# Performance work log

Measured on AMD Instinct MI355X. Metric: run time of the kernel, lower is better.

The kernel has to match this reference:

```python
import jax, jax.numpy as jnp
import numpy as np

B, N, DIM, H = 8, 1024, 768, 12
D = DIM // H  # head_dim = 64
SCALE = D ** -0.5


def setup_inputs() -> dict:
    key = jax.random.key(0)
    k1, k2, k3, k4 = jax.random.split(key, 4)
    x = jax.random.normal(k1, (B, N, DIM), dtype=jnp.float32)
    # nn.Linear(dim, dim*3, bias=False): weight [3*dim, dim]; y = x @ W^T
    w_qkv = jax.random.normal(k2, (3 * DIM, DIM), dtype=jnp.float32) * (DIM ** -0.5)
    # nn.Linear(dim, dim) with bias
    w_proj = jax.random.normal(k3, (DIM, DIM), dtype=jnp.float32) * (DIM ** -0.5)
    b_proj = jax.random.normal(k4, (DIM,), dtype=jnp.float32) * 0.01
    return {"x": x, "w_qkv": w_qkv, "w_proj": w_proj, "b_proj": b_proj}


def reference(x, w_qkv, w_proj, b_proj):
    b, n, dim = x.shape
    qkv = x @ w_qkv.T  # [b, n, 3*dim]
    # rearrange 'b n (h d qkv) -> qkv b h n d' (qkv innermost in the split)
    qkv = qkv.reshape(b, n, H, D, 3)
    qkv = jnp.transpose(qkv, (4, 0, 2, 1, 3))  # [3, b, h, n, d]
    q, k, v = qkv[0], qkv[1], qkv[2]
    energy = jnp.einsum('bhqd,bhkd->bhqk', q, k) * SCALE
    att = jax.nn.softmax(energy, axis=-1)  # dropout p=0.0 -> identity
    out = jnp.einsum('bhal,bhlv->bhav', att, v)  # [b, h, n, d]
    out = jnp.transpose(out, (0, 2, 1, 3)).reshape(b, n, dim)
    return out @ w_proj.T + b_proj
```

## Files before the change

kernel.cpp:

```cpp
#include <hip/hip_runtime.h>
#include <hip/hip_bf16.h>
#include <stdint.h>

#define NH 12

typedef __attribute__((ext_vector_type(8))) short bf16x8;
typedef __attribute__((ext_vector_type(4))) float f32x4;

static __device__ __forceinline__ ushort f2bf(float f) {
  union { float f; uint32_t u; } v; v.f = f;
  uint32_t r = (v.u + 0x7FFFu + ((v.u >> 16) & 1u)) >> 16;
  return (ushort)r;
}

static __device__ __forceinline__ uint32_t cvtpk(float lo, float hi) {
  uint32_t r;
  asm("v_cvt_pk_bf16_f32 %0, %1, %2" : "=v"(r) : "v"(lo), "v"(hi));
  return r;
}

static __device__ __forceinline__ void gl_lds16(const void* g, void* l) {
  __builtin_amdgcn_global_load_lds(
      (const __attribute__((address_space(1))) uint32_t*)(uintptr_t)g,
      (__attribute__((address_space(3))) uint32_t*)(uintptr_t)l,
      16, 0, 0);
}

static __device__ __forceinline__ f32x4 mfma32(bf16x8 a, bf16x8 b, f32x4 c) {
  return __builtin_amdgcn_mfma_f32_16x16x32_bf16(a, b, c, 0, 0, 0);
}

#define QSCALE 0.1803368801111601f

#define N4_X  1572864
#define N4_WQ 442368
#define N4_WP 147456
__global__ __launch_bounds__(256) void k_cvt_all(const float4* __restrict__ X,
                                                 const float4* __restrict__ Wq,
                                                 const float4* __restrict__ Wp,
                                                 ushort4* __restrict__ Xb,
                                                 ushort4* __restrict__ Wqb,
                                                 ushort4* __restrict__ Wpb) {
  int i = blockIdx.x * 256 + threadIdx.x;
  if (i < N4_X) {
    float4 v = X[i];
    ushort4 o;
    o.x = f2bf(v.x); o.y = f2bf(v.y); o.z = f2bf(v.z); o.w = f2bf(v.w);
    Xb[i] = o;
  } else if (i < N4_X + N4_WQ) {
    int j = i - N4_X;
    int ro = j / 192, cc = j - ro * 192;
    int h = ro / 192;
    int rem = ro - h * 192;
    int d = rem / 3;
    int which = rem - d * 3;
    int rn = which * 768 + h * 64 + d;
    float4 v = Wq[j];
    ushort4 o;
    o.x = f2bf(v.x); o.y = f2bf(v.y); o.z = f2bf(v.z); o.w = f2bf(v.w);
    Wqb[(size_t)rn * 192 + cc] = o;
  } else {
    int j = i - N4_X - N4_WQ;
    float4 v = Wp[j];
    ushort4 o;
    o.x = f2bf(v.x); o.y = f2bf(v.y); o.z = f2bf(v.z); o.w = f2bf(v.w);
    Wpb[j] = o;
  }
}

#define DECL_GEMM_VARS() \
  const int tid = threadIdx.x; \
  const int w = tid >> 6, l = tid & 63, g = l >> 4, c15 = l & 15; \
  const int wm = w >> 1, wn = w & 1; \
  const int dst0 = w * 1024 + l * 16; \
  const int row_s = w * 16 + (l >> 2); \
  const int cg = ((l & 3) ^ ((l >> 3) & 3)) * 8; \
  const int gsw = (g ^ ((c15 >> 1) & 3)) * 8;

#define STAGE(pa, pb, Aptr, Bptr, kk0) do { \
    gl_lds16((Aptr) + (size_t)(m0 + row_s) * 768 + (kk0) + cg, (char*)(pa) + dst0); \
    gl_lds16((Aptr) + (size_t)(m0 + row_s + 64) * 768 + (kk0) + cg, (char*)(pa) + dst0 + 4096); \
    gl_lds16((Bptr) + (size_t)(n0 + row_s) * 768 + (kk0) + cg, (char*)(pb) + dst0); \
    gl_lds16((Bptr) + (size_t)(n0 + row_s + 64) * 768 + (kk0) + cg, (char*)(pb) + dst0 + 4096); \
  } while (0)

#define COMPUTE(pa, pb) do { \
    bf16x8 af[4], bfr[4]; \
    _Pragma("unroll") \
    for (int i = 0; i < 4; i++) { \
      af[i]  = *(const bf16x8*)&(pa)[(wm * 64 + i * 16 + c15) * 32 + gsw]; \
      bfr[i] = *(const bf16x8*)&(pb)[(wn * 64 + i * 16 + c15) * 32 + gsw]; \
    } \
    _Pragma("unroll") \
    for (int mr = 0; mr < 4; mr++) \
      _Pragma("unroll") \
      for (int nr = 0; nr < 4; nr++) \
        acc[mr][nr] = mfma32(af[mr], bfr[nr], acc[mr][nr]); \
  } while (0)

#define WB4 do { __builtin_amdgcn_sched_barrier(0); \
    asm volatile("s_waitcnt vmcnt(4)\n\ts_barrier" ::: "memory"); \
    __builtin_amdgcn_sched_barrier(0); } while (0)
#define WB2 do { __builtin_amdgcn_sched_barrier(0); \
    asm volatile("s_waitcnt vmcnt(2)\n\ts_barrier" ::: "memory"); \
    __builtin_amdgcn_sched_barrier(0); } while (0)
#define WB0 do { __builtin_amdgcn_sched_barrier(0); \
    asm volatile("s_waitcnt vmcnt(0)\n\ts_barrier" ::: "memory"); \
    __builtin_amdgcn_sched_barrier(0); } while (0)
#define PFENCE do { asm volatile("" ::: "memory"); \
    __builtin_amdgcn_sched_barrier(0); } while (0)

#define GEMM_PIPE(Aptr, Bptr) do { \
    STAGE(A0, B0, Aptr, Bptr, 0); \
    PFENCE; \
    STAGE(A1, B1, Aptr, Bptr, 32); \
    WB4; \
    _Pragma("unroll 1") \
    for (int k0 = 0; k0 < 672; k0 += 96) { \
      STAGE(A2, B2, Aptr, Bptr, k0 + 64);  COMPUTE(A0, B0); WB4; \
      STAGE(A0, B0, Aptr, Bptr, k0 + 96);  COMPUTE(A1, B1); WB4; \
      STAGE(A1, B1, Aptr, Bptr, k0 + 128); COMPUTE(A2, B2); WB4; \
    } \
    STAGE(A2, B2, Aptr, Bptr, 736); COMPUTE(A0, B0); WB4; \
    COMPUTE(A1, B1); WB0; \
    COMPUTE(A2, B2); \
  } while (0)

__global__ __launch_bounds__(256, 3) void k_qkv(const ushort* __restrict__ X,
                                                const ushort* __restrict__ W,
                                                ushort* __restrict__ Qb,
                                                ushort* __restrict__ Kf,
                                                ushort* __restrict__ Vf) {
  __shared__ __align__(16) ushort lds[24576];
  const int id = (int)blockIdx.x;
  const int swz = (id & 7) * 144 + (id >> 3);
  const int bx = swz % 18, by = swz / 18;
  const int m0 = by * 128, n0 = bx * 128;
  DECL_GEMM_VARS();

  ushort* A0 = lds;
  ushort* A1 = lds + 4096;
  ushort* A2 = lds + 8192;
  ushort* B0 = lds + 12288;
  ushort* B1 = lds + 16384;
  ushort* B2 = lds + 20480;

  f32x4 acc[4][4] = {};
  GEMM_PIPE(X, W);
  __syncthreads();

  const int type = bx / 6;
  const int cb = (bx % 6) * 128;
  const int h0 = cb >> 6;
  const int b = m0 >> 10, nbase = m0 & 1023, tbase = nbase >> 5;

  if (type == 0) {
#pragma unroll
    for (int nr = 0; nr < 4; nr++) {
      const int colrel = wn * 64 + nr * 16 + c15;
#pragma unroll
      for (int mr = 0; mr < 4; mr++)
#pragma unroll
        for (int r = 0; r < 4; r++) {
          const int mrel = wm * 64 + mr * 16 + 4 * g + r;
          lds[mrel * 128 + colrel] = f2bf(acc[mr][nr][r] * QSCALE);
        }
    }
    __syncthreads();
#pragma unroll
    for (int j = 0; j < 8; j++) {
      const int cid = j * 256 + tid;
      const int n = cid >> 4, coloff = (cid & 15) * 8;
      const int hrel = coloff >> 6, d0q = coloff & 63;
      bf16x8 vv = *(const bf16x8*)&lds[n * 128 + coloff];
      *(bf16x8*)(Qb + ((size_t)(b * NH + h0 + hrel) * 1024 + nbase + n) * 64 + d0q) = vv;
    }
  } else if (type == 1) {
#pragma unroll
    for (int nr = 0; nr < 4; nr++) {
      const int colrel = wn * 64 + nr * 16 + c15;
      const int hrel = colrel >> 6, d = colrel & 63;
      const int gk = (d >> 3) & 3, ek = d & 7, hi = d >> 5;
#pragma unroll
      for (int mr = 0; mr < 4; mr++)
#pragma unroll
        for (int r = 0; r < 4; r++) {
          const int mrel = wm * 64 + mr * 16 + 4 * g + r;
          const int trel = mrel >> 5, kk = mrel & 31;
          const int x = kk >> 3, s = (kk >> 2) & 1, y = kk & 3;
          lds[(hrel * 4 + trel) * 2048 + (2 * s + hi) * 512 +
              (gk * 16 + x * 4 + y) * 8 + ek] = f2bf(acc[mr][nr][r]);
        }
    }
    __syncthreads();
    const int c = tid >> 5, jj = tid & 31;
    ushort* dst = Kf + ((size_t)(b * NH + h0 + (c >> 2)) * 32 + tbase + (c & 3)) * 2048;
    const ushort* srcl = lds + c * 2048;
#pragma unroll
    for (int k2 = 0; k2 < 8; k2++)
      *(bf16x8*)(dst + jj * 8 + k2 * 256) = *(const bf16x8*)(srcl + jj * 8 + k2 * 256);
  } else {
#pragma unroll
    for (int nr = 0; nr < 4; nr++) {
      const int colrel = wn * 64 + nr * 16 + c15;
      const int hrel = colrel >> 6, d = colrel & 63;
      const int dtv = d >> 4, cv = d & 15;
#pragma unroll
      for (int mr = 0; mr < 4; mr++)
#pragma unroll
        for (int r = 0; r < 4; r++) {
          const int mrel = wm * 64 + mr * 16 + 4 * g + r;
          const int trel = mrel >> 5, kk = mrel & 31;
          const int gv = kk >> 3, ev = kk & 7;
          lds[(hrel * 4 + trel) * 2048 + dtv * 512 +
              (gv * 16 + cv) * 8 + ev] = f2bf(acc[mr][nr][r]);
        }
    }
    __syncthreads();
    const int c = tid >> 5, jj = tid & 31;
    ushort* dst = Vf + ((size_t)(b * NH + h0 + (c >> 2)) * 32 + tbase + (c & 3)) * 2048;
    const ushort* srcl = lds + c * 2048;
#pragma unroll
    for (int k2 = 0; k2 < 8; k2++)
      *(bf16x8*)(dst + jj * 8 + k2 * 256) = *(const bf16x8*)(srcl + jj * 8 + k2 * 256);
  }
}

__global__ __launch_bounds__(256, 3) void k_attn(const ushort* __restrict__ Qb,
                                                 const ushort* __restrict__ Kf,
                                                 const ushort* __restrict__ Vf,
                                                 ushort* __restrict__ Ab) {
  __shared__ __align__(16) ushort kv[3][4096];
  const int bh = blockIdx.x;
  const int tid = threadIdx.x;
  const int w = tid >> 6, l = tid & 63, g = l >> 4, c15 = l & 15;
  const int q0 = blockIdx.y * 128 + w * 32;

  bf16x8 qf0a, qf0b, qf1a, qf1b;
  {
    const ushort* qp = Qb + ((size_t)bh * 1024 + q0 + c15) * 64 + g * 8;
    qf0a = *(const bf16x8*)qp;
    qf0b = *(const bf16x8*)(qp + 32);
    qf1a = *(const bf16x8*)(qp + 1024);
    qf1b = *(const bf16x8*)(qp + 1024 + 32);
  }
  const ushort* kgb = Kf + (size_t)bh * 32 * 2048;
  const ushort* vgb = Vf + (size_t)bh * 32 * 2048;

  bf16x8 vones;
#pragma unroll
  for (int j = 0; j < 8; j++) vones[j] = (short)0x3F80;

  f32x4 o0[4] = {}, o1[4] = {};
  f32x4 ol0 = {}, ol1 = {};

#define STAGE_KV(bi, t) do { \
    gl_lds16(kgb + (size_t)(t) * 2048 + tid * 8, (char*)kv[bi] + tid * 16); \
    gl_lds16(vgb + (size_t)(t) * 2048 + tid * 8, (char*)kv[bi] + 4096 + tid * 16); \
  } while (0)

#define ATT_BODY(bi) do { \
    const ushort* kp = kv[bi] + l * 8; \
    const ushort* vp = kv[bi] + 2048 + l * 8; \
    bf16x8 ka0a = *(const bf16x8*)(kp); \
    bf16x8 ka0b = *(const bf16x8*)(kp + 512); \
    bf16x8 ka1a = *(const bf16x8*)(kp + 1024); \
    bf16x8 ka1b = *(const bf16x8*)(kp + 1536); \
    f32x4 s00 = {0.f,0.f,0.f,0.f}, s01 = {0.f,0.f,0.f,0.f}; \
    f32x4 s10 = {0.f,0.f,0.f,0.f}, s11 = {0.f,0.f,0.f,0.f}; \
    s00 = mfma32(ka0a, qf0a, s00); s00 = mfma32(ka0b, qf0b, s00); \
    s01 = mfma32(ka0a, qf1a, s01); s01 = mfma32(ka0b, qf1b, s01); \
    s10 = mfma32(ka1a, qf0a, s10); s10 = mfma32(ka1b, qf0b, s10); \
    s11 = mfma32(ka1a, qf1a, s11); s11 = mfma32(ka1b, qf1b, s11); \
    float p0[8], p1[8]; \
    _Pragma("unroll") \
    for (int r = 0; r < 4; r++) { \
      p0[r]     = exp2f(s00[r]); \
      p0[4 + r] = exp2f(s10[r]); \
      p1[r]     = exp2f(s01[r]); \
      p1[4 + r] = exp2f(s11[r]); \
    } \
    union { uint32_t u[4]; bf16x8 v; } pa0, pa1; \
    _Pragma("unroll") \
    for (int j = 0; j < 4; j++) { \
      pa0.u[j] = cvtpk(p0[2 * j], p0[2 * j + 1]); \
      pa1.u[j] = cvtpk(p1[2 * j], p1[2 * j + 1]); \
    } \
    ol0 = mfma32(pa0.v, vones, ol0); \
    ol1 = mfma32(pa1.v, vones, ol1); \
    _Pragma("unroll") \
    for (int dt = 0; dt < 4; dt++) { \
      bf16x8 vb = *(const bf16x8*)(vp + dt * 512); \
      o0[dt] = mfma32(pa0.v, vb, o0[dt]); \
      o1[dt] = mfma32(pa1.v, vb, o1[dt]); \
    } \
  } while (0)

  STAGE_KV(0, 0);
  PFENCE;
  STAGE_KV(1, 1);
  WB2;
#pragma unroll 1
  for (int t = 0; t < 27; t += 3) {
    STAGE_KV(2, t + 2); ATT_BODY(0); WB2;
    STAGE_KV(0, t + 3); ATT_BODY(1); WB2;
    STAGE_KV(1, t + 4); ATT_BODY(2); WB2;
  }
  STAGE_KV(2, 29); ATT_BODY(0); WB2;
  STAGE_KV(0, 30); ATT_BODY(1); WB2;
  STAGE_KV(1, 31); ATT_BODY(2); WB2;
  ATT_BODY(0); WB0;
  ATT_BODY(1);
#undef ATT_BODY
#undef STAGE_KV

  float il0[4], il1[4];
#pragma unroll
  for (int r = 0; r < 4; r++) {
    il0[r] = __builtin_amdgcn_rcpf(ol0[r]);
    il1[r] = __builtin_amdgcn_rcpf(ol1[r]);
  }
  const int b = bh / NH, h = bh % NH;
#pragma unroll
  for (int dt = 0; dt < 4; dt++)
#pragma unroll
    for (int r = 0; r < 4; r++) {
      const int n = q0 + 4 * g + r;
      Ab[(size_t)(b * 1024 + n) * 768 + h * 64 + dt * 16 + c15] =
          f2bf(o0[dt][r] * il0[r]);
      Ab[(size_t)(b * 1024 + n + 16) * 768 + h * 64 + dt * 16 + c15] =
          f2bf(o1[dt][r] * il1[r]);
    }
}

__global__ __launch_bounds__(256, 3) void k_proj(const ushort* __restrict__ Ain,
                                                 const ushort* __restrict__ W,
                                                 const float* __restrict__ Bp,
                                                 float* __restrict__ Out) {
  __shared__ __align__(16) ushort lds[24576];
  const int id = (int)blockIdx.x;
  const int swz = (id & 7) * 48 + (id >> 3);
  const int bx = swz % 6, by = swz / 6;
  const int m0 = by * 128, n0 = bx * 128;
  DECL_GEMM_VARS();

  ushort* A0 = lds;
  ushort* A1 = lds + 4096;
  ushort* A2 = lds + 8192;
  ushort* B0 = lds + 12288;
  ushort* B1 = lds + 16384;
  ushort* B2 = lds + 20480;

  f32x4 acc[4][4] = {};
  GEMM_PIPE(Ain, W);

#pragma unroll
  for (int nr = 0; nr < 4; nr++) {
    const int cc = n0 + wn * 64 + nr * 16 + c15;
    const float bias = Bp[cc];
#pragma unroll
    for (int mr = 0; mr < 4; mr++) {
      const int mb = m0 + wm * 64 + mr * 16 + 4 * g;
#pragma unroll
      for (int r = 0; r < 4; r++) {
        const int m = mb + r;
        Out[(size_t)m * 768 + cc] = acc[mr][nr][r] + bias;
      }
    }
  }
}

extern "C" void kernel_launch(void* const* d_in, const int* in_sizes, int n_in,
                              void* d_out, int out_size, void* d_ws, size_t ws_size,
                              hipStream_t stream) {
  const float* X  = (const float*)d_in[0];
  const float* Wq = (const float*)d_in[1];
  const float* Wp = (const float*)d_in[2];
  const float* Bp = (const float*)d_in[3];
  float* Out = (float*)d_out;

  char* ws = (char*)d_ws;
  const size_t SZ = (size_t)96 * 1024 * 64 * sizeof(ushort);
  ushort* Qb  = (ushort*)(ws);
  ushort* Kf  = (ushort*)(ws + SZ);
  ushort* Vf  = (ushort*)(ws + 2 * SZ);
  ushort* Ab  = (ushort*)(ws + 3 * SZ);
  ushort* Xb  = (ushort*)(ws + 4 * SZ);
  ushort* Wqb = (ushort*)(ws + 5 * SZ);
  ushort* Wpb = (ushort*)(ws + 5 * SZ + 2304 * 768 * 2);

  k_cvt_all<<<(N4_X + N4_WQ + N4_WP) / 256, 256, 0, stream>>>(
      (const float4*)X, (const float4*)Wq, (const float4*)Wp,
      (ushort4*)Xb, (ushort4*)Wqb, (ushort4*)Wpb);

  k_qkv<<<1152, 256, 0, stream>>>(Xb, Wqb, Qb, Kf, Vf);
  k_attn<<<dim3(96, 8), 256, 0, stream>>>(Qb, Kf, Vf, Ab);
  k_proj<<<384, 256, 0, stream>>>(Ab, Wpb, Bp, Out);
}
```

Measured before the change: 108.6 us.

## Load A fragments directly to registers and quad-buffer B in LDS

The two GEMM kernels now load the A operand straight from global memory into register fragments with double-buffered registers, and stage only the B operand into LDS through a 4-slot ring. This shrinks LDS per block from 48KB to 32KB, and launch bounds are raised to 4 blocks per CU. The aim is to cut LDS traffic and raise occupancy. In exchange, the direct A loads are 16-byte per-lane global loads with a 1536-byte row stride, so they coalesce less well and hide latency less. Register pressure also rises from holding the extra fragments.

Measured after the change: 175.6 us. 61.7% more time.

```diff
diff --git a/kernel.cpp b/kernel.cpp
--- a/kernel.cpp
+++ b/kernel.cpp
@@ -77,20 +77,24 @@
   const int cg = ((l & 3) ^ ((l >> 3) & 3)) * 8; \
   const int gsw = (g ^ ((c15 >> 1) & 3)) * 8;
 
-#define STAGE(pa, pb, Aptr, Bptr, kk0) do { \
-    gl_lds16((Aptr) + (size_t)(m0 + row_s) * 768 + (kk0) + cg, (char*)(pa) + dst0); \
-    gl_lds16((Aptr) + (size_t)(m0 + row_s + 64) * 768 + (kk0) + cg, (char*)(pa) + dst0 + 4096); \
-    gl_lds16((Bptr) + (size_t)(n0 + row_s) * 768 + (kk0) + cg, (char*)(pb) + dst0); \
-    gl_lds16((Bptr) + (size_t)(n0 + row_s + 64) * 768 + (kk0) + cg, (char*)(pb) + dst0 + 4096); \
-  } while (0)
-
-#define COMPUTE(pa, pb) do { \
-    bf16x8 af[4], bfr[4]; \
-    _Pragma("unroll") \
-    for (int i = 0; i < 4; i++) { \
-      af[i]  = *(const bf16x8*)&(pa)[(wm * 64 + i * 16 + c15) * 32 + gsw]; \
-      bfr[i] = *(const bf16x8*)&(pb)[(wn * 64 + i * 16 + c15) * 32 + gsw]; \
-    } \
+#define B_STAGE(bi, Bptr, kk0) do { \
+    char* _b = (char*)lds + (bi) * 8192; \
+    gl_lds16((Bptr) + (size_t)(n0 + row_s) * 768 + (kk0) + cg, _b + dst0); \
+    gl_lds16((Bptr) + (size_t)(n0 + row_s + 64) * 768 + (kk0) + cg, _b + dst0 + 4096); \
+  } while (0)
+
+#define A_LOAD(af, Aptr, kk0) do { \
+    _Pragma("unroll") \
+    for (int i = 0; i < 4; i++) \
+      af[i] = *(const bf16x8*)((Aptr) + (size_t)(m0 + wm * 64 + i * 16 + c15) * 768 + (kk0) + g * 8); \
+  } while (0)
+
+#define COMPUTE2(af, bi) do { \
+    const ushort* _bb = lds + (bi) * 4096; \
+    bf16x8 bfr[4]; \
+    _Pragma("unroll") \
+    for (int i = 0; i < 4; i++) \
+      bfr[i] = *(const bf16x8*)&_bb[(wn * 64 + i * 16 + c15) * 32 + gsw]; \
     _Pragma("unroll") \
     for (int mr = 0; mr < 4; mr++) \
       _Pragma("unroll") \
@@ -98,6 +102,9 @@
         acc[mr][nr] = mfma32(af[mr], bfr[nr], acc[mr][nr]); \
   } while (0)
 
+#define WB6 do { __builtin_amdgcn_sched_barrier(0); \
+    asm volatile("s_waitcnt vmcnt(6)\n\ts_barrier" ::: "memory"); \
+    __builtin_amdgcn_sched_barrier(0); } while (0)
 #define WB4 do { __builtin_amdgcn_sched_barrier(0); \
     asm volatile("s_waitcnt vmcnt(4)\n\ts_barrier" ::: "memory"); \
     __builtin_amdgcn_sched_barrier(0); } while (0)
@@ -110,43 +117,43 @@
 #define PFENCE do { asm volatile("" ::: "memory"); \
     __builtin_amdgcn_sched_barrier(0); } while (0)
 
-#define GEMM_PIPE(Aptr, Bptr) do { \
-    STAGE(A0, B0, Aptr, Bptr, 0); \
-    PFENCE; \
-    STAGE(A1, B1, Aptr, Bptr, 32); \
+#define GEMM_PIPE2(Aptr, Bptr) do { \
+    B_STAGE(0, Bptr, 0); PFENCE; \
+    B_STAGE(1, Bptr, 32); PFENCE; \
+    A_LOAD(afA, Aptr, 0); PFENCE; \
+    _Pragma("unroll 1") \
+    for (int p = 0; p < 22; p += 2) { \
+      B_STAGE((p + 2) & 3, Bptr, (p + 2) * 32); \
+      A_LOAD(afB, Aptr, (p + 1) * 32); \
+      WB6; \
+      COMPUTE2(afA, p & 3); \
+      B_STAGE((p + 3) & 3, Bptr, (p + 3) * 32); \
+      A_LOAD(afA, Aptr, (p + 2) * 32); \
+      WB6; \
+      COMPUTE2(afB, (p + 1) & 3); \
+    } \
+    A_LOAD(afB, Aptr, 736); \
     WB4; \
-    _Pragma("unroll 1") \
-    for (int k0 = 0; k0 < 672; k0 += 96) { \
-      STAGE(A2, B2, Aptr, Bptr, k0 + 64);  COMPUTE(A0, B0); WB4; \
-      STAGE(A0, B0, Aptr, Bptr, k0 + 96);  COMPUTE(A1, B1); WB4; \
-      STAGE(A1, B1, Aptr, Bptr, k0 + 128); COMPUTE(A2, B2); WB4; \
-    } \
-    STAGE(A2, B2, Aptr, Bptr, 736); COMPUTE(A0, B0); WB4; \
-    COMPUTE(A1, B1); WB0; \
-    COMPUTE(A2, B2); \
-  } while (0)
-
-__global__ __launch_bounds__(256, 3) void k_qkv(const ushort* __restrict__ X,
+    COMPUTE2(afA, 2); \
+    WB0; \
+    COMPUTE2(afB, 3); \
+  } while (0)
+
+__global__ __launch_bounds__(256, 4) void k_qkv(const ushort* __restrict__ X,
                                                 const ushort* __restrict__ W,
                                                 ushort* __restrict__ Qb,
                                                 ushort* __restrict__ Kf,
                                                 ushort* __restrict__ Vf) {
-  __shared__ __align__(16) ushort lds[24576];
+  __shared__ __align__(16) ushort lds[16384];
   const int id = (int)blockIdx.x;
   const int swz = (id & 7) * 144 + (id >> 3);
   const int bx = swz % 18, by = swz / 18;
   const int m0 = by * 128, n0 = bx * 128;
   DECL_GEMM_VARS();
 
-  ushort* A0 = lds;
-  ushort* A1 = lds + 4096;
-  ushort* A2 = lds + 8192;
-  ushort* B0 = lds + 12288;
-  ushort* B1 = lds + 16384;
-  ushort* B2 = lds + 20480;
-
   f32x4 acc[4][4] = {};
-  GEMM_PIPE(X, W);
+  bf16x8 afA[4], afB[4];
+  GEMM_PIPE2(X, W);
   __syncthreads();
 
   const int type = bx / 6;
@@ -333,26 +340,20 @@
     }
 }
 
-__global__ __launch_bounds__(256, 3) void k_proj(const ushort* __restrict__ Ain,
+__global__ __launch_bounds__(256, 4) void k_proj(const ushort* __restrict__ Ain,
                                                  const ushort* __restrict__ W,
                                                  const float* __restrict__ Bp,
                                                  float* __restrict__ Out) {
-  __shared__ __align__(16) ushort lds[24576];
+  __shared__ __align__(16) ushort lds[16384];
   const int id = (int)blockIdx.x;
   const int swz = (id & 7) * 48 + (id >> 3);
   const int bx = swz % 6, by = swz / 6;
   const int m0 = by * 128, n0 = bx * 128;
   DECL_GEMM_VARS();
 
-  ushort* A0 = lds;
-  ushort* A1 = lds + 4096;
-  ushort* A2 = lds + 8192;
-  ushort* B0 = lds + 12288;
-  ushort* B1 = lds + 16384;
-  ushort* B2 = lds + 20480;
-
   f32x4 acc[4][4] = {};
-  GEMM_PIPE(Ain, W);
+  bf16x8 afA[4], afB[4];
+  GEMM_PIPE2(Ain, W);
 
 #pragma unroll
   for (int nr = 0; nr < 4; nr++) {
```

## Retile QKV GEMM to 256x128 blocks with 8 waves sharing B fragments

Applied to the files above, without the earlier changes.

The QKV projection kernel now uses 512-thread blocks that each compute a 256x128 output tile. Each of the 8 waves owns 32 rows and all 128 columns, so the B tile is loaded once per block and shared across more rows, halving the grid to 576 blocks. The staging pipeline is rewritten to move three 16-byte loads per thread per k-step, and the epilogue is adapted to the taller tile. LDS use grows to 72KB per block and each wave now issues more B-fragment LDS reads, which may limit occupancy. The attention kernel is only moved in the file, unchanged.

Measured after the change: 111.3 us. 1.02x slower.

```diff
diff --git a/kernel.cpp b/kernel.cpp
--- a/kernel.cpp
+++ b/kernel.cpp
@@ -68,38 +68,11 @@
   }
 }
 
-#define DECL_GEMM_VARS() \
-  const int tid = threadIdx.x; \
-  const int w = tid >> 6, l = tid & 63, g = l >> 4, c15 = l & 15; \
-  const int wm = w >> 1, wn = w & 1; \
-  const int dst0 = w * 1024 + l * 16; \
-  const int row_s = w * 16 + (l >> 2); \
-  const int cg = ((l & 3) ^ ((l >> 3) & 3)) * 8; \
-  const int gsw = (g ^ ((c15 >> 1) & 3)) * 8;
-
-#define STAGE(pa, pb, Aptr, Bptr, kk0) do { \
-    gl_lds16((Aptr) + (size_t)(m0 + row_s) * 768 + (kk0) + cg, (char*)(pa) + dst0); \
-    gl_lds16((Aptr) + (size_t)(m0 + row_s + 64) * 768 + (kk0) + cg, (char*)(pa) + dst0 + 4096); \
-    gl_lds16((Bptr) + (size_t)(n0 + row_s) * 768 + (kk0) + cg, (char*)(pb) + dst0); \
-    gl_lds16((Bptr) + (size_t)(n0 + row_s + 64) * 768 + (kk0) + cg, (char*)(pb) + dst0 + 4096); \
-  } while (0)
-
-#define COMPUTE(pa, pb) do { \
-    bf16x8 af[4], bfr[4]; \
-    _Pragma("unroll") \
-    for (int i = 0; i < 4; i++) { \
-      af[i]  = *(const bf16x8*)&(pa)[(wm * 64 + i * 16 + c15) * 32 + gsw]; \
-      bfr[i] = *(const bf16x8*)&(pb)[(wn * 64 + i * 16 + c15) * 32 + gsw]; \
-    } \
-    _Pragma("unroll") \
-    for (int mr = 0; mr < 4; mr++) \
-      _Pragma("unroll") \
-      for (int nr = 0; nr < 4; nr++) \
-        acc[mr][nr] = mfma32(af[mr], bfr[nr], acc[mr][nr]); \
-  } while (0)
-
 #define WB4 do { __builtin_amdgcn_sched_barrier(0); \
     asm volatile("s_waitcnt vmcnt(4)\n\ts_barrier" ::: "memory"); \
+    __builtin_amdgcn_sched_barrier(0); } while (0)
+#define WB3 do { __builtin_amdgcn_sched_barrier(0); \
+    asm volatile("s_waitcnt vmcnt(3)\n\ts_barrier" ::: "memory"); \
     __builtin_amdgcn_sched_barrier(0); } while (0)
 #define WB2 do { __builtin_amdgcn_sched_barrier(0); \
     asm volatile("s_waitcnt vmcnt(2)\n\ts_barrier" ::: "memory"); \
@@ -109,6 +82,283 @@
     __builtin_amdgcn_sched_barrier(0); } while (0)
 #define PFENCE do { asm volatile("" ::: "memory"); \
     __builtin_amdgcn_sched_barrier(0); } while (0)
+
+__global__ __launch_bounds__(512, 4) void k_qkv(const ushort* __restrict__ X,
+                                                const ushort* __restrict__ W,
+                                                ushort* __restrict__ Qb,
+                                                ushort* __restrict__ Kf,
+                                                ushort* __restrict__ Vf) {
+  __shared__ __align__(16) ushort lds[36864];
+  const int id = (int)blockIdx.x;
+  const int swz = (id & 7) * 72 + (id >> 3);
+  const int bx = swz % 18, by = swz / 18;
+  const int m0 = by * 256, n0 = bx * 128;
+  const int tid = threadIdx.x;
+  const int w = tid >> 6, l = tid & 63, g = l >> 4, c15 = l & 15;
+  const int rowA = tid >> 2;
+  const int cgA = ((tid & 3) ^ ((tid >> 3) & 3)) * 8;
+  const int gsw = (g ^ ((c15 >> 1) & 3)) * 8;
+
+#define A_BUF(i) ((char*)lds + (i) * 16384)
+#define B_BUF(i) ((char*)lds + 49152 + (i) * 8192)
+
+#define STAGE8(bi, kk0) do { \
+    gl_lds16(X + (size_t)(m0 + rowA) * 768 + (kk0) + cgA, A_BUF(bi) + tid * 16); \
+    gl_lds16(X + (size_t)(m0 + rowA + 128) * 768 + (kk0) + cgA, A_BUF(bi) + tid * 16 + 8192); \
+    gl_lds16(W + (size_t)(n0 + rowA) * 768 + (kk0) + cgA, B_BUF(bi) + tid * 16); \
+  } while (0)
+
+#define COMPUTE8(bi) do { \
+    const ushort* _a = (const ushort*)A_BUF(bi); \
+    const ushort* _b = (const ushort*)B_BUF(bi); \
+    bf16x8 af[2], bfr[8]; \
+    _Pragma("unroll") \
+    for (int i = 0; i < 2; i++) \
+      af[i] = *(const bf16x8*)&_a[(w * 32 + i * 16 + c15) * 32 + gsw]; \
+    _Pragma("unroll") \
+    for (int i = 0; i < 8; i++) \
+      bfr[i] = *(const bf16x8*)&_b[(i * 16 + c15) * 32 + gsw]; \
+    _Pragma("unroll") \
+    for (int mr = 0; mr < 2; mr++) \
+      _Pragma("unroll") \
+      for (int nr = 0; nr < 8; nr++) \
+        acc[mr][nr] = mfma32(af[mr], bfr[nr], acc[mr][nr]); \
+  } while (0)
+
+  f32x4 acc[2][8] = {};
+
+  STAGE8(0, 0);
+  PFENCE;
+  STAGE8(1, 32);
+  WB3;
+#pragma unroll 1
+  for (int p = 0; p < 21; p += 3) {
+    STAGE8(2, (p + 2) * 32); COMPUTE8(0); WB3;
+    STAGE8(0, (p + 3) * 32); COMPUTE8(1); WB3;
+    STAGE8(1, (p + 4) * 32); COMPUTE8(2); WB3;
+  }
+  STAGE8(2, 736); COMPUTE8(0); WB3;
+  COMPUTE8(1); WB0;
+  COMPUTE8(2);
+  __syncthreads();
+
+  const int type = bx / 6;
+  const int cb = (bx % 6) * 128;
+  const int h0 = cb >> 6;
+  const int b = m0 >> 10, nbase = m0 & 1023, tbase = nbase >> 5;
+
+  if (type == 0) {
+#pragma unroll
+    for (int nr = 0; nr < 8; nr++) {
+      const int colrel = nr * 16 + c15;
+#pragma unroll
+      for (int mr = 0; mr < 2; mr++)
+#pragma unroll
+        for (int r = 0; r < 4; r++) {
+          const int mrel = w * 32 + mr * 16 + 4 * g + r;
+          lds[mrel * 128 + colrel] = f2bf(acc[mr][nr][r] * QSCALE);
+        }
+    }
+    __syncthreads();
+#pragma unroll
+    for (int j = 0; j < 8; j++) {
+      const int cid = j * 512 + tid;
+      const int n = cid >> 4, coloff = (cid & 15) * 8;
+      const int hrel = coloff >> 6, d0q = coloff & 63;
+      bf16x8 vv = *(const bf16x8*)&lds[n * 128 + coloff];
+      *(bf16x8*)(Qb + ((size_t)(b * NH + h0 + hrel) * 1024 + nbase + n) * 64 + d0q) = vv;
+    }
+  } else if (type == 1) {
+#pragma unroll
+    for (int nr = 0; nr < 8; nr++) {
+      const int colrel = nr * 16 + c15;
+      const int hrel = colrel >> 6, d = colrel & 63;
+      const int gk = (d >> 3) & 3, ek = d & 7, hi = d >> 5;
+#pragma unroll
+      for (int mr = 0; mr < 2; mr++)
+#pragma unroll
+        for (int r = 0; r < 4; r++) {
+          const int mrel = w * 32 + mr * 16 + 4 * g + r;
+          const int trel = mrel >> 5, kk = mrel & 31;
+          const int x = kk >> 3, s = (kk >> 2) & 1, y = kk & 3;
+          lds[(hrel * 8 + trel) * 2048 + (2 * s + hi) * 512 +
+              (gk * 16 + x * 4 + y) * 8 + ek] = f2bf(acc[mr][nr][r]);
+        }
+    }
+    __syncthreads();
+    const int c = tid >> 5, jj = tid & 31;
+    ushort* dst = Kf + ((size_t)(b * NH + h0 + (c >> 3)) * 32 + tbase + (c & 7)) * 2048;
+    const ushort* srcl = lds + c * 2048;
+#pragma unroll
+    for (int k2 = 0; k2 < 8; k2++)
+      *(bf16x8*)(dst + jj * 8 + k2 * 256) = *(const bf16x8*)(srcl + jj * 8 + k2 * 256);
+  } else {
+#pragma unroll
+    for (int nr = 0; nr < 8; nr++) {
+      const int colrel = nr * 16 + c15;
+      const int hrel = colrel >> 6, d = colrel & 63;
+      const int dtv = d >> 4, cv = d & 15;
+#pragma unroll
+      for (int mr = 0; mr < 2; mr++)
+#pragma unroll
+        for (int r = 0; r < 4; r++) {
+          const int mrel = w * 32 + mr * 16 + 4 * g + r;
+          const int trel = mrel >> 5, kk = mrel & 31;
+          const int gv = kk >> 3, ev = kk & 7;
+          lds[(hrel * 8 + trel) * 2048 + dtv * 512 +
+              (gv * 16 + cv) * 8 + ev] = f2bf(acc[mr][nr][r]);
+        }
+    }
+    __syncthreads();
+    const int c = tid >> 5, jj = tid & 31;
+    ushort* dst = Vf + ((size_t)(b * NH + h0 + (c >> 3)) * 32 + tbase + (c & 7)) * 2048;
+    const ushort* srcl = lds + c * 2048;
+#pragma unroll
+    for (int k2 = 0; k2 < 8; k2++)
+      *(bf16x8*)(dst + jj * 8 + k2 * 256) = *(const bf16x8*)(srcl + jj * 8 + k2 * 256);
+  }
+#undef STAGE8
+#undef COMPUTE8
+#undef A_BUF
+#undef B_BUF
+}
+
+__global__ __launch_bounds__(256, 3) void k_attn(const ushort* __restrict__ Qb,
+                                                 const ushort* __restrict__ Kf,
+                                                 const ushort* __restrict__ Vf,
+                                                 ushort* __restrict__ Ab) {
+  __shared__ __align__(16) ushort kv[3][4096];
+  const int bh = blockIdx.x;
+  const int tid = threadIdx.x;
+  const int w = tid >> 6, l = tid & 63, g = l >> 4, c15 = l & 15;
+  const int q0 = blockIdx.y * 128 + w * 32;
+
+  bf16x8 qf0a, qf0b, qf1a, qf1b;
+  {
+    const ushort* qp = Qb + ((size_t)bh * 1024 + q0 + c15) * 64 + g * 8;
+    qf0a = *(const bf16x8*)qp;
+    qf0b = *(const bf16x8*)(qp + 32);
+    qf1a = *(const bf16x8*)(qp + 1024);
+    qf1b = *(const bf16x8*)(qp + 1024 + 32);
+  }
+  const ushort* kgb = Kf + (size_t)bh * 32 * 2048;
+  const ushort* vgb = Vf + (size_t)bh * 32 * 2048;
+
+  bf16x8 vones;
+#pragma unroll
+  for (int j = 0; j < 8; j++) vones[j] = (short)0x3F80;
+
+  f32x4 o0[4] = {}, o1[4] = {};
+  f32x4 ol0 = {}, ol1 = {};
+
+#define STAGE_KV(bi, t) do { \
+    gl_lds16(kgb + (size_t)(t) * 2048 + tid * 8, (char*)kv[bi] + tid * 16); \
+    gl_lds16(vgb + (size_t)(t) * 2048 + tid * 8, (char*)kv[bi] + 4096 + tid * 16); \
+  } while (0)
+
+#define ATT_BODY(bi) do { \
+    const ushort* kp = kv[bi] + l * 8; \
+    const ushort* vp = kv[bi] + 2048 + l * 8; \
+    bf16x8 ka0a = *(const bf16x8*)(kp); \
+    bf16x8 ka0b = *(const bf16x8*)(kp + 512); \
+    bf16x8 ka1a = *(const bf16x8*)(kp + 1024); \
+    bf16x8 ka1b = *(const bf16x8*)(kp + 1536); \
+    f32x4 s00 = {0.f,0.f,0.f,0.f}, s01 = {0.f,0.f,0.f,0.f}; \
+    f32x4 s10 = {0.f,0.f,0.f,0.f}, s11 = {0.f,0.f,0.f,0.f}; \
+    s00 = mfma32(ka0a, qf0a, s00); s00 = mfma32(ka0b, qf0b, s00); \
+    s01 = mfma32(ka0a, qf1a, s01); s01 = mfma32(ka0b, qf1b, s01); \
+    s10 = mfma32(ka1a, qf0a, s10); s10 = mfma32(ka1b, qf0b, s10); \
+    s11 = mfma32(ka1a, qf1a, s11); s11 = mfma32(ka1b, qf1b, s11); \
+    float p0[8], p1[8]; \
+    _Pragma("unroll") \
+    for (int r = 0; r < 4; r++) { \
+      p0[r]     = exp2f(s00[r]); \
+      p0[4 + r] = exp2f(s10[r]); \
+      p1[r]     = exp2f(s01[r]); \
+      p1[4 + r] = exp2f(s11[r]); \
+    } \
+    union { uint32_t u[4]; bf16x8 v; } pa0, pa1; \
+    _Pragma("unroll") \
+    for (int j = 0; j < 4; j++) { \
+      pa0.u[j] = cvtpk(p0[2 * j], p0[2 * j + 1]); \
+      pa1.u[j] = cvtpk(p1[2 * j], p1[2 * j + 1]); \
+    } \
+    ol0 = mfma32(pa0.v, vones, ol0); \
+    ol1 = mfma32(pa1.v, vones, ol1); \
+    _Pragma("unroll") \
+    for (int dt = 0; dt < 4; dt++) { \
+      bf16x8 vb = *(const bf16x8*)(vp + dt * 512); \
+      o0[dt] = mfma32(pa0.v, vb, o0[dt]); \
+      o1[dt] = mfma32(pa1.v, vb, o1[dt]); \
+    } \
+  } while (0)
+
+  STAGE_KV(0, 0);
+  PFENCE;
+  STAGE_KV(1, 1);
+  WB2;
+#pragma unroll 1
+  for (int t = 0; t < 27; t += 3) {
+    STAGE_KV(2, t + 2); ATT_BODY(0); WB2;
+    STAGE_KV(0, t + 3); ATT_BODY(1); WB2;
+    STAGE_KV(1, t + 4); ATT_BODY(2); WB2;
+  }
+  STAGE_KV(2, 29); ATT_BODY(0); WB2;
+  STAGE_KV(0, 30); ATT_BODY(1); WB2;
+  STAGE_KV(1, 31); ATT_BODY(2); WB2;
+  ATT_BODY(0); WB0;
+  ATT_BODY(1);
+#undef ATT_BODY
+#undef STAGE_KV
+
+  float il0[4], il1[4];
+#pragma unroll
+  for (int r = 0; r < 4; r++) {
+    il0[r] = __builtin_amdgcn_rcpf(ol0[r]);
+    il1[r] = __builtin_amdgcn_rcpf(ol1[r]);
+  }
+  const int b = bh / NH, h = bh % NH;
+#pragma unroll
+  for (int dt = 0; dt < 4; dt++)
+#pragma unroll
+    for (int r = 0; r < 4; r++) {
+      const int n = q0 + 4 * g + r;
+      Ab[(size_t)(b * 1024 + n) * 768 + h * 64 + dt * 16 + c15] =
+          f2bf(o0[dt][r] * il0[r]);
+      Ab[(size_t)(b * 1024 + n + 16) * 768 + h * 64 + dt * 16 + c15] =
+          f2bf(o1[dt][r] * il1[r]);
+    }
+}
+
+#define DECL_GEMM_VARS() \
+  const int tid = threadIdx.x; \
+  const int w = tid >> 6, l = tid & 63, g = l >> 4, c15 = l & 15; \
+  const int wm = w >> 1, wn = w & 1; \
+  const int dst0 = w * 1024 + l * 16; \
+  const int row_s = w * 16 + (l >> 2); \
+  const int cg = ((l & 3) ^ ((l >> 3) & 3)) * 8; \
+  const int gsw = (g ^ ((c15 >> 1) & 3)) * 8;
+
+#define STAGE(pa, pb, Aptr, Bptr, kk0) do { \
+    gl_lds16((Aptr) + (size_t)(m0 + row_s) * 768 + (kk0) + cg, (char*)(pa) + dst0); \
+    gl_lds16((Aptr) + (size_t)(m0 + row_s + 64) * 768 + (kk0) + cg, (char*)(pa) + dst0 + 4096); \
+    gl_lds16((Bptr) + (size_t)(n0 + row_s) * 768 + (kk0) + cg, (char*)(pb) + dst0); \
+    gl_lds16((Bptr) + (size_t)(n0 + row_s + 64) * 768 + (kk0) + cg, (char*)(pb) + dst0 + 4096); \
+  } while (0)
+
+#define COMPUTE(pa, pb) do { \
+    bf16x8 af[4], bfr[4]; \
+    _Pragma("unroll") \
+    for (int i = 0; i < 4; i++) { \
+      af[i]  = *(const bf16x8*)&(pa)[(wm * 64 + i * 16 + c15) * 32 + gsw]; \
+      bfr[i] = *(const bf16x8*)&(pb)[(wn * 64 + i * 16 + c15) * 32 + gsw]; \
+    } \
+    _Pragma("unroll") \
+    for (int mr = 0; mr < 4; mr++) \
+      _Pragma("unroll") \
+      for (int nr = 0; nr < 4; nr++) \
+        acc[mr][nr] = mfma32(af[mr], bfr[nr], acc[mr][nr]); \
+  } while (0)
 
 #define GEMM_PIPE(Aptr, Bptr) do { \
     STAGE(A0, B0, Aptr, Bptr, 0); \
@@ -126,213 +376,6 @@
     COMPUTE(A2, B2); \
   } while (0)
 
-__global__ __launch_bounds__(256, 3) void k_qkv(const ushort* __restrict__ X,
-                                                const ushort* __restrict__ W,
-                                                ushort* __restrict__ Qb,
-                                                ushort* __restrict__ Kf,
-                                                ushort* __restrict__ Vf) {
-  __shared__ __align__(16) ushort lds[24576];
-  const int id = (int)blockIdx.x;
-  const int swz = (id & 7) * 144 + (id >> 3);
-  const int bx = swz % 18, by = swz / 18;
-  const int m0 = by * 128, n0 = bx * 128;
-  DECL_GEMM_VARS();
-
-  ushort* A0 = lds;
-  ushort* A1 = lds + 4096;
-  ushort* A2 = lds + 8192;
-  ushort* B0 = lds + 12288;
-  ushort* B1 = lds + 16384;
-  ushort* B2 = lds + 20480;
-
-  f32x4 acc[4][4] = {};
-  GEMM_PIPE(X, W);
-  __syncthreads();
-
-  const int type = bx / 6;
-  const int cb = (bx % 6) * 128;
-  const int h0 = cb >> 6;
-  const int b = m0 >> 10, nbase = m0 & 1023, tbase = nbase >> 5;
-
-  if (type == 0) {
-#pragma unroll
-    for (int nr = 0; nr < 4; nr++) {
-      const int colrel = wn * 64 + nr * 16 + c15;
-#pragma unroll
-      for (int mr = 0; mr < 4; mr++)
-#pragma unroll
-        for (int r = 0; r < 4; r++) {
-          const int mrel = wm * 64 + mr * 16 + 4 * g + r;
-          lds[mrel * 128 + colrel] = f2bf(acc[mr][nr][r] * QSCALE);
-        }
-    }
-    __syncthreads();
-#pragma unroll
-    for (int j = 0; j < 8; j++) {
-      const int cid = j * 256 + tid;
-      const int n = cid >> 4, coloff = (cid & 15) * 8;
-      const int hrel = coloff >> 6, d0q = coloff & 63;
-      bf16x8 vv = *(const bf16x8*)&lds[n * 128 + coloff];
-      *(bf16x8*)(Qb + ((size_t)(b * NH + h0 + hrel) * 1024 + nbase + n) * 64 + d0q) = vv;
-    }
-  } else if (type == 1) {
-#pragma unroll
-    for (int nr = 0; nr < 4; nr++) {
-      const int colrel = wn * 64 + nr * 16 + c15;
-      const int hrel = colrel >> 6, d = colrel & 63;
-      const int gk = (d >> 3) & 3, ek = d & 7, hi = d >> 5;
-#pragma unroll
-      for (int mr = 0; mr < 4; mr++)
-#pragma unroll
-        for (int r = 0; r < 4; r++) {
-          const int mrel = wm * 64 + mr * 16 + 4 * g + r;
-          const int trel = mrel >> 5, kk = mrel & 31;
-          const int x = kk >> 3, s = (kk >> 2) & 1, y = kk & 3;
-          lds[(hrel * 4 + trel) * 2048 + (2 * s + hi) * 512 +
-              (gk * 16 + x * 4 + y) * 8 + ek] = f2bf(acc[mr][nr][r]);
-        }
-    }
-    __syncthreads();
-    const int c = tid >> 5, jj = tid & 31;
-    ushort* dst = Kf + ((size_t)(b * NH + h0 + (c >> 2)) * 32 + tbase + (c & 3)) * 2048;
-    const ushort* srcl = lds + c * 2048;
-#pragma unroll
-    for (int k2 = 0; k2 < 8; k2++)
-      *(bf16x8*)(dst + jj * 8 + k2 * 256) = *(const bf16x8*)(srcl + jj * 8 + k2 * 256);
-  } else {
-#pragma unroll
-    for (int nr = 0; nr < 4; nr++) {
-      const int colrel = wn * 64 + nr * 16 + c15;
-      const int hrel = colrel >> 6, d = colrel & 63;
-      const int dtv = d >> 4, cv = d & 15;
-#pragma unroll
-      for (int mr = 0; mr < 4; mr++)
-#pragma unroll
-        for (int r = 0; r < 4; r++) {
-          const int mrel = wm * 64 + mr * 16 + 4 * g + r;
-          const int trel = mrel >> 5, kk = mrel & 31;
-          const int gv = kk >> 3, ev = kk & 7;
-          lds[(hrel * 4 + trel) * 2048 + dtv * 512 +
-              (gv * 16 + cv) * 8 + ev] = f2bf(acc[mr][nr][r]);
-        }
-    }
-    __syncthreads();
-    const int c = tid >> 5, jj = tid & 31;
-    ushort* dst = Vf + ((size_t)(b * NH + h0 + (c >> 2)) * 32 + tbase + (c & 3)) * 2048;
-    const ushort* srcl = lds + c * 2048;
-#pragma unroll
-    for (int k2 = 0; k2 < 8; k2++)
-      *(bf16x8*)(dst + jj * 8 + k2 * 256) = *(const bf16x8*)(srcl + jj * 8 + k2 * 256);
-  }
-}
-
-__global__ __launch_bounds__(256, 3) void k_attn(const ushort* __restrict__ Qb,
-                                                 const ushort* __restrict__ Kf,
-                                                 const ushort* __restrict__ Vf,
-                                                 ushort* __restrict__ Ab) {
-  __shared__ __align__(16) ushort kv[3][4096];
-  const int bh = blockIdx.x;
-  const int tid = threadIdx.x;
-  const int w = tid >> 6, l = tid & 63, g = l >> 4, c15 = l & 15;
-  const int q0 = blockIdx.y * 128 + w * 32;
-
-  bf16x8 qf0a, qf0b, qf1a, qf1b;
-  {
-    const ushort* qp = Qb + ((size_t)bh * 1024 + q0 + c15) * 64 + g * 8;
-    qf0a = *(const bf16x8*)qp;
-    qf0b = *(const bf16x8*)(qp + 32);
-    qf1a = *(const bf16x8*)(qp + 1024);
-    qf1b = *(const bf16x8*)(qp + 1024 + 32);
-  }
-  const ushort* kgb = Kf + (size_t)bh * 32 * 2048;
-  const ushort* vgb = Vf + (size_t)bh * 32 * 2048;
-
-  bf16x8 vones;
-#pragma unroll
-  for (int j = 0; j < 8; j++) vones[j] = (short)0x3F80;
-
-  f32x4 o0[4] = {}, o1[4] = {};
-  f32x4 ol0 = {}, ol1 = {};
-
-#define STAGE_KV(bi, t) do { \
-    gl_lds16(kgb + (size_t)(t) * 2048 + tid * 8, (char*)kv[bi] + tid * 16); \
-    gl_lds16(vgb + (size_t)(t) * 2048 + tid * 8, (char*)kv[bi] + 4096 + tid * 16); \
-  } while (0)
-
-#define ATT_BODY(bi) do { \
-    const ushort* kp = kv[bi] + l * 8; \
-    const ushort* vp = kv[bi] + 2048 + l * 8; \
-    bf16x8 ka0a = *(const bf16x8*)(kp); \
-    bf16x8 ka0b = *(const bf16x8*)(kp + 512); \
-    bf16x8 ka1a = *(const bf16x8*)(kp + 1024); \
-    bf16x8 ka1b = *(const bf16x8*)(kp + 1536); \
-    f32x4 s00 = {0.f,0.f,0.f,0.f}, s01 = {0.f,0.f,0.f,0.f}; \
-    f32x4 s10 = {0.f,0.f,0.f,0.f}, s11 = {0.f,0.f,0.f,0.f}; \
-    s00 = mfma32(ka0a, qf0a, s00); s00 = mfma32(ka0b, qf0b, s00); \
-    s01 = mfma32(ka0a, qf1a, s01); s01 = mfma32(ka0b, qf1b, s01); \
-    s10 = mfma32(ka1a, qf0a, s10); s10 = mfma32(ka1b, qf0b, s10); \
-    s11 = mfma32(ka1a, qf1a, s11); s11 = mfma32(ka1b, qf1b, s11); \
-    float p0[8], p1[8]; \
-    _Pragma("unroll") \
-    for (int r = 0; r < 4; r++) { \
-      p0[r]     = exp2f(s00[r]); \
-      p0[4 + r] = exp2f(s10[r]); \
-      p1[r]     = exp2f(s01[r]); \
-      p1[4 + r] = exp2f(s11[r]); \
-    } \
-    union { uint32_t u[4]; bf16x8 v; } pa0, pa1; \
-    _Pragma("unroll") \
-    for (int j = 0; j < 4; j++) { \
-      pa0.u[j] = cvtpk(p0[2 * j], p0[2 * j + 1]); \
-      pa1.u[j] = cvtpk(p1[2 * j], p1[2 * j + 1]); \
-    } \
-    ol0 = mfma32(pa0.v, vones, ol0); \
-    ol1 = mfma32(pa1.v, vones, ol1); \
-    _Pragma("unroll") \
-    for (int dt = 0; dt < 4; dt++) { \
-      bf16x8 vb = *(const bf16x8*)(vp + dt * 512); \
-      o0[dt] = mfma32(pa0.v, vb, o0[dt]); \
-      o1[dt] = mfma32(pa1.v, vb, o1[dt]); \
-    } \
-  } while (0)
-
-  STAGE_KV(0, 0);
-  PFENCE;
-  STAGE_KV(1, 1);
-  WB2;
-#pragma unroll 1
-  for (int t = 0; t < 27; t += 3) {
-    STAGE_KV(2, t + 2); ATT_BODY(0); WB2;
-    STAGE_KV(0, t + 3); ATT_BODY(1); WB2;
-    STAGE_KV(1, t + 4); ATT_BODY(2); WB2;
-  }
-  STAGE_KV(2, 29); ATT_BODY(0); WB2;
-  STAGE_KV(0, 30); ATT_BODY(1); WB2;
-  STAGE_KV(1, 31); ATT_BODY(2); WB2;
-  ATT_BODY(0); WB0;
-  ATT_BODY(1);
-#undef ATT_BODY
-#undef STAGE_KV
-
-  float il0[4], il1[4];
-#pragma unroll
-  for (int r = 0; r < 4; r++) {
-    il0[r] = __builtin_amdgcn_rcpf(ol0[r]);
-    il1[r] = __builtin_amdgcn_rcpf(ol1[r]);
-  }
-  const int b = bh / NH, h = bh % NH;
-#pragma unroll
-  for (int dt = 0; dt < 4; dt++)
-#pragma unroll
-    for (int r = 0; r < 4; r++) {
-      const int n = q0 + 4 * g + r;
-      Ab[(size_t)(b * 1024 + n) * 768 + h * 64 + dt * 16 + c15] =
-          f2bf(o0[dt][r] * il0[r]);
-      Ab[(size_t)(b * 1024 + n + 16) * 768 + h * 64 + dt * 16 + c15] =
-          f2bf(o1[dt][r] * il1[r]);
-    }
-}
-
 __global__ __launch_bounds__(256, 3) void k_proj(const ushort* __restrict__ Ain,
                                                  const ushort* __restrict__ W,
                                                  const float* __restrict__ Bp,
@@ -393,7 +436,7 @@
       (const float4*)X, (const float4*)Wq, (const float4*)Wp,
       (ushort4*)Xb, (ushort4*)Wqb, (ushort4*)Wpb);
 
-  k_qkv<<<1152, 256, 0, stream>>>(Xb, Wqb, Qb, Kf, Vf);
+  k_qkv<<<576, 512, 0, stream>>>(Xb, Wqb, Qb, Kf, Vf);
   k_attn<<<dim3(96, 8), 256, 0, stream>>>(Qb, Kf, Vf, Ab);
   k_proj<<<384, 256, 0, stream>>>(Ab, Wpb, Bp, Out);
 }
```

## Fuse X fp32-to-bf16 conversion into QKV GEMM register-staged A loads

Applied to the files above, without the earlier changes.

Removes the separate conversion pass over the input activations. The QKV GEMM now loads fp32 X directly into registers, converts it to bf16 with packed converts, and writes it into LDS, while B (weights) still uses direct global-to-LDS loads. This saves a full write and re-read of the bf16 X buffer. In exchange, the GEMM reads twice as many A bytes, uses more registers, and adds LDS stores and extra waitcnt synchronization to the pipelined loop.

Result: no change. 109.6 us (+0.9%).

```diff
diff --git a/kernel.cpp b/kernel.cpp
--- a/kernel.cpp
+++ b/kernel.cpp
@@ -32,23 +32,15 @@
 
 #define QSCALE 0.1803368801111601f
 
-#define N4_X  1572864
 #define N4_WQ 442368
 #define N4_WP 147456
-__global__ __launch_bounds__(256) void k_cvt_all(const float4* __restrict__ X,
-                                                 const float4* __restrict__ Wq,
-                                                 const float4* __restrict__ Wp,
-                                                 ushort4* __restrict__ Xb,
-                                                 ushort4* __restrict__ Wqb,
-                                                 ushort4* __restrict__ Wpb) {
+__global__ __launch_bounds__(256) void k_cvt_w(const float4* __restrict__ Wq,
+                                               const float4* __restrict__ Wp,
+                                               ushort4* __restrict__ Wqb,
+                                               ushort4* __restrict__ Wpb) {
   int i = blockIdx.x * 256 + threadIdx.x;
-  if (i < N4_X) {
-    float4 v = X[i];
-    ushort4 o;
-    o.x = f2bf(v.x); o.y = f2bf(v.y); o.z = f2bf(v.z); o.w = f2bf(v.w);
-    Xb[i] = o;
-  } else if (i < N4_X + N4_WQ) {
-    int j = i - N4_X;
+  if (i < N4_WQ) {
+    int j = i;
     int ro = j / 192, cc = j - ro * 192;
     int h = ro / 192;
     int rem = ro - h * 192;
@@ -59,8 +51,8 @@
     ushort4 o;
     o.x = f2bf(v.x); o.y = f2bf(v.y); o.z = f2bf(v.z); o.w = f2bf(v.w);
     Wqb[(size_t)rn * 192 + cc] = o;
-  } else {
-    int j = i - N4_X - N4_WQ;
+  } else if (i < N4_WQ + N4_WP) {
+    int j = i - N4_WQ;
     float4 v = Wp[j];
     ushort4 o;
     o.x = f2bf(v.x); o.y = f2bf(v.y); o.z = f2bf(v.z); o.w = f2bf(v.w);
@@ -108,6 +100,13 @@
     asm volatile("s_waitcnt vmcnt(0)\n\ts_barrier" ::: "memory"); \
     __builtin_amdgcn_sched_barrier(0); } while (0)
 #define PFENCE do { asm volatile("" ::: "memory"); \
+    __builtin_amdgcn_sched_barrier(0); } while (0)
+
+#define WBP do { __builtin_amdgcn_sched_barrier(0); \
+    asm volatile("s_waitcnt vmcnt(6) lgkmcnt(0)\n\ts_barrier" ::: "memory"); \
+    __builtin_amdgcn_sched_barrier(0); } while (0)
+#define WBT do { __builtin_amdgcn_sched_barrier(0); \
+    asm volatile("s_waitcnt vmcnt(0) lgkmcnt(0)\n\ts_barrier" ::: "memory"); \
     __builtin_amdgcn_sched_barrier(0); } while (0)
 
 #define GEMM_PIPE(Aptr, Bptr) do { \
@@ -126,7 +125,7 @@
     COMPUTE(A2, B2); \
   } while (0)
 
-__global__ __launch_bounds__(256, 3) void k_qkv(const ushort* __restrict__ X,
+__global__ __launch_bounds__(256, 3) void k_qkv(const float* __restrict__ Xf,
                                                 const ushort* __restrict__ W,
                                                 ushort* __restrict__ Qb,
                                                 ushort* __restrict__ Kf,
@@ -146,7 +145,67 @@
   ushort* B2 = lds + 20480;
 
   f32x4 acc[4][4] = {};
-  GEMM_PIPE(X, W);
+  float4 ra0, ra1, ra2, ra3, rb0, rb1, rb2, rb3;
+
+#define AISSUE(r0, r1, r2, r3, kk) do { \
+    const float* _p = Xf + (size_t)(m0 + row_s) * 768 + (kk) + cg; \
+    r0 = *(const float4*)_p; \
+    r1 = *(const float4*)(_p + 4); \
+    const float* _q = _p + (size_t)64 * 768; \
+    r2 = *(const float4*)_q; \
+    r3 = *(const float4*)(_q + 4); \
+  } while (0)
+
+#define BSTAGE(pb, kk) do { \
+    gl_lds16(W + (size_t)(n0 + row_s) * 768 + (kk) + cg, (char*)(pb) + dst0); \
+    gl_lds16(W + (size_t)(n0 + row_s + 64) * 768 + (kk) + cg, (char*)(pb) + dst0 + 4096); \
+  } while (0)
+
+#define AWRITE(Abuf, r0, r1, r2, r3) do { \
+    union { uint32_t u[4]; bf16x8 v; } _w0, _w1; \
+    _w0.u[0] = cvtpk(r0.x, r0.y); _w0.u[1] = cvtpk(r0.z, r0.w); \
+    _w0.u[2] = cvtpk(r1.x, r1.y); _w0.u[3] = cvtpk(r1.z, r1.w); \
+    _w1.u[0] = cvtpk(r2.x, r2.y); _w1.u[1] = cvtpk(r2.z, r2.w); \
+    _w1.u[2] = cvtpk(r3.x, r3.y); _w1.u[3] = cvtpk(r3.z, r3.w); \
+    *(bf16x8*)((char*)(Abuf) + tid * 16) = _w0.v; \
+    *(bf16x8*)((char*)(Abuf) + tid * 16 + 4096) = _w1.v; \
+  } while (0)
+
+  AISSUE(ra0, ra1, ra2, ra3, 0);
+  BSTAGE(B0, 0);
+  PFENCE;
+  AISSUE(rb0, rb1, rb2, rb3, 32);
+  BSTAGE(B1, 32);
+  AWRITE(A0, ra0, ra1, ra2, ra3);
+  WBP;
+#pragma unroll 1
+  for (int k0 = 0; k0 < 576; k0 += 192) {
+    AISSUE(ra0, ra1, ra2, ra3, k0 + 64);  BSTAGE(B2, k0 + 64);
+    AWRITE(A1, rb0, rb1, rb2, rb3); COMPUTE(A0, B0); WBP;
+    AISSUE(rb0, rb1, rb2, rb3, k0 + 96);  BSTAGE(B0, k0 + 96);
+    AWRITE(A2, ra0, ra1, ra2, ra3); COMPUTE(A1, B1); WBP;
+    AISSUE(ra0, ra1, ra2, ra3, k0 + 128); BSTAGE(B1, k0 + 128);
+    AWRITE(A0, rb0, rb1, rb2, rb3); COMPUTE(A2, B2); WBP;
+    AISSUE(rb0, rb1, rb2, rb3, k0 + 160); BSTAGE(B2, k0 + 160);
+    AWRITE(A1, ra0, ra1, ra2, ra3); COMPUTE(A0, B0); WBP;
+    AISSUE(ra0, ra1, ra2, ra3, k0 + 192); BSTAGE(B0, k0 + 192);
+    AWRITE(A2, rb0, rb1, rb2, rb3); COMPUTE(A1, B1); WBP;
+    AISSUE(rb0, rb1, rb2, rb3, k0 + 224); BSTAGE(B1, k0 + 224);
+    AWRITE(A0, ra0, ra1, ra2, ra3); COMPUTE(A2, B2); WBP;
+  }
+  AISSUE(ra0, ra1, ra2, ra3, 640); BSTAGE(B2, 640);
+  AWRITE(A1, rb0, rb1, rb2, rb3); COMPUTE(A0, B0); WBP;
+  AISSUE(rb0, rb1, rb2, rb3, 672); BSTAGE(B0, 672);
+  AWRITE(A2, ra0, ra1, ra2, ra3); COMPUTE(A1, B1); WBP;
+  AISSUE(ra0, ra1, ra2, ra3, 704); BSTAGE(B1, 704);
+  AWRITE(A0, rb0, rb1, rb2, rb3); COMPUTE(A2, B2); WBP;
+  AISSUE(rb0, rb1, rb2, rb3, 736); BSTAGE(B2, 736);
+  AWRITE(A1, ra0, ra1, ra2, ra3); COMPUTE(A0, B0); WBP;
+  AWRITE(A2, rb0, rb1, rb2, rb3); COMPUTE(A1, B1); WBT;
+  COMPUTE(A2, B2);
+#undef AISSUE
+#undef BSTAGE
+#undef AWRITE
   __syncthreads();
 
   const int type = bx / 6;
@@ -385,15 +444,13 @@
   ushort* Kf  = (ushort*)(ws + SZ);
   ushort* Vf  = (ushort*)(ws + 2 * SZ);
   ushort* Ab  = (ushort*)(ws + 3 * SZ);
-  ushort* Xb  = (ushort*)(ws + 4 * SZ);
-  ushort* Wqb = (ushort*)(ws + 5 * SZ);
-  ushort* Wpb = (ushort*)(ws + 5 * SZ + 2304 * 768 * 2);
-
-  k_cvt_all<<<(N4_X + N4_WQ + N4_WP) / 256, 256, 0, stream>>>(
-      (const float4*)X, (const float4*)Wq, (const float4*)Wp,
-      (ushort4*)Xb, (ushort4*)Wqb, (ushort4*)Wpb);
-
-  k_qkv<<<1152, 256, 0, stream>>>(Xb, Wqb, Qb, Kf, Vf);
+  ushort* Wqb = (ushort*)(ws + 4 * SZ);
+  ushort* Wpb = (ushort*)(ws + 4 * SZ + 2304 * 768 * 2);
+
+  k_cvt_w<<<(N4_WQ + N4_WP + 255) / 256, 256, 0, stream>>>(
+      (const float4*)Wq, (const float4*)Wp, (ushort4*)Wqb, (ushort4*)Wpb);
+
+  k_qkv<<<1152, 256, 0, stream>>>(X, Wqb, Qb, Kf, Vf);
   k_attn<<<dim3(96, 8), 256, 0, stream>>>(Qb, Kf, Vf, Ab);
   k_proj<<<384, 256, 0, stream>>>(Ab, Wpb, Bp, Out);
 }
```
